# Performance work log

Hardware: AMD Instinct MI355X
Metric: run time of the kernel (lower is better)

Reference implementation:

```python
import jax, jax.numpy as jnp
import numpy as np

TOPK = 50
TEMP = 5.0

def _l2norm(x):
    return x / jnp.linalg.norm(x, axis=-1, keepdims=True)

def setup_inputs() -> dict:
    key = jax.random.key(0)
    k1, k2, k3 = jax.random.split(key, 3)
    b, m, d = 32, 196, 512
    n, c = 51, 1000
    return {
        "image_features": jax.random.normal(k1, (b, d), dtype=jnp.float32),
        "local_image_features": jax.random.normal(k2, (b, m, d), dtype=jnp.float32),
        "all_text_features": jax.random.normal(k3, (n, c, d), dtype=jnp.float32),
        "logit_scale": jnp.full((1,), 4.6052, dtype=jnp.float32),  # ln(100), CLIP default
    }

def reference(image_features, local_image_features, all_text_features, logit_scale):
    # Inference path of CustomCLIP.forward (labels=None) -> get_dense_logits2
    img = _l2norm(image_features)                 # [b, d]
    loc = _l2norm(local_image_features)           # [b, m, d]
    txt = _l2norm(all_text_features)              # [n, c, d]  (n = ndisc = 51)
    mean_txt = _l2norm(txt.mean(axis=0))          # [c, d]

    base_logits = img @ mean_txt.T                # [b, c]
    w_raw = jnp.einsum('bd,bmd->bm', img, loc)    # [b, m]
    txt_cnd = jnp.transpose(txt, (1, 0, 2))       # [c, n, d]
    v = jax.nn.softmax(jnp.einsum('cd,cnd->cn', mean_txt, txt_cnd) * TEMP, axis=1)  # [c, n]

    # similarity of every patch to every description, laid out with m last for top_k
    sim = jnp.einsum('bmd,cnd->bcnm', loc, txt_cnd)        # [b, c, n, m]
    sim_topk, idx_topk = jax.lax.top_k(sim, TOPK)          # [b, c, n, k] each

    b = img.shape[0]
    # gather per-image patch weights at selected patch indices: w_raw[b, idx]
    w_topk = w_raw[jnp.arange(b)[:, None, None, None], idx_topk]   # [b, c, n, k]
    w = jax.nn.softmax(w_topk * TEMP, axis=3)               # softmax over selected patches

    bias_logits = jnp.sum(sim_topk * w * v[None, :, :, None], axis=(2, 3))  # [b, c]
    return jnp.exp(logit_scale)[0] * (base_logits + bias_logits)
```

## Files before the change

kernel.cpp:

```cpp
#include <hip/hip_runtime.h>
#include <stdint.h>

typedef __bf16  bf16x8 __attribute__((ext_vector_type(8)));
typedef float   f32x4  __attribute__((ext_vector_type(4)));
typedef short   s16x2  __attribute__((ext_vector_type(2)));
typedef unsigned short u16;

#define TEMP 5.0f

__device__ inline float wsum(float v){
  #pragma unroll
  for (int off=32; off; off>>=1) v += __shfl_xor(v, off, 64);
  return v;
}
__device__ inline float wmax(float v){
  #pragma unroll
  for (int off=32; off; off>>=1) v = fmaxf(v, __shfl_xor(v, off, 64));
  return v;
}
__device__ inline u16 f2bf(float f){
  unsigned u = __float_as_uint(f);
  u = u + 0x7fffu + ((u>>16)&1u);
  return (u16)(u>>16);
}
__device__ inline float bfl(unsigned u){ return __uint_as_float(u<<16); }
__device__ inline float bfh(unsigned u){ return __uint_as_float(u & 0xffff0000u); }

__device__ inline s16x2 as_s16x2(int v){ union{int i; s16x2 v;} u; u.i=v; return u.v; }

__device__ inline s16x2 pkmin2(s16x2 a, s16x2 b){
  s16x2 r; r.x = a.x < b.x ? a.x : b.x; r.y = a.y < b.y ? a.y : b.y; return r;
}
__device__ inline s16x2 pkmax2(s16x2 a, s16x2 b){
  s16x2 r; r.x = a.x > b.x ? a.x : b.x; r.y = a.y > b.y ? a.y : b.y; return r;
}

#if __has_builtin(__builtin_amdgcn_mov_dpp)
__device__ inline int dxor1(int v){ return __builtin_amdgcn_mov_dpp(v, 0xB1, 0xF, 0xF, true); }
__device__ inline int dxor2(int v){ return __builtin_amdgcn_mov_dpp(v, 0x4E, 0xF, 0xF, true); }
#else
__device__ inline int dxor1(int v){ return __shfl_xor(v, 1, 64); }
__device__ inline int dxor2(int v){ return __shfl_xor(v, 2, 64); }
#endif

#if __has_builtin(__builtin_amdgcn_permlane16_swap)
__device__ inline int x16sum_i(int c){
  auto p = __builtin_amdgcn_permlane16_swap((unsigned)c, (unsigned)c, false, false);
  return (int)p[0] + (int)p[1];
}
__device__ inline int x16min_i(int c){
  auto p = __builtin_amdgcn_permlane16_swap((unsigned)c, (unsigned)c, false, false);
  return min((int)p[0], (int)p[1]);
}
__device__ inline int x16max_i(int c){
  auto p = __builtin_amdgcn_permlane16_swap((unsigned)c, (unsigned)c, false, false);
  return max((int)p[0], (int)p[1]);
}
__device__ inline float x16sum_f(float v){
  auto p = __builtin_amdgcn_permlane16_swap(__float_as_uint(v), __float_as_uint(v), false, false);
  return __uint_as_float(p[0]) + __uint_as_float(p[1]);
}
#else
__device__ inline int   x16sum_i(int c){ return c + __shfl_xor(c, 16, 64); }
__device__ inline int   x16min_i(int c){ return min(c, __shfl_xor(c, 16, 64)); }
__device__ inline int   x16max_i(int c){ return max(c, __shfl_xor(c, 16, 64)); }
__device__ inline float x16sum_f(float v){ return v + __shfl_xor(v, 16, 64); }
#endif

__device__ inline int ssum8_i(int c){ c += dxor1(c); c += dxor2(c); return x16sum_i(c); }
__device__ inline int smin8_i(int c){ c = min(c, dxor1(c)); c = min(c, dxor2(c)); return x16min_i(c); }
__device__ inline int smax8_i(int c){ c = max(c, dxor1(c)); c = max(c, dxor2(c)); return x16max_i(c); }
__device__ inline float ssum8_f(float v){
  v += __int_as_float(dxor1(__float_as_int(v)));
  v += __int_as_float(dxor2(__float_as_int(v)));
  return x16sum_f(v);
}

__device__ inline void cp16(void* lds_uniform, const void* g){
  __builtin_amdgcn_global_load_lds(
    (const __attribute__((address_space(1))) unsigned int*)g,
    (__attribute__((address_space(3))) unsigned int*)lds_uniform, 16, 0, 0);
}

__global__ void k_img(const float* __restrict__ X, float* __restrict__ imgn){
  int b = blockIdx.x, lane = threadIdx.x;
  const float* src = X + (size_t)b*512 + lane*8;
  float4 a = *(const float4*)src;
  float4 c = *(const float4*)(src+4);
  float ss = a.x*a.x+a.y*a.y+a.z*a.z+a.w*a.w + c.x*c.x+c.y*c.y+c.z*c.z+c.w*c.w;
  ss = wsum(ss);
  float inv = 1.0f/sqrtf(ss);
  float* dst = imgn + (size_t)b*512 + lane*8;
  float4 o0 = {a.x*inv,a.y*inv,a.z*inv,a.w*inv};
  float4 o1 = {c.x*inv,c.y*inv,c.z*inv,c.w*inv};
  *(float4*)dst = o0; *(float4*)(dst+4) = o1;
}

__global__ void k_txt(const float* __restrict__ X, u16* __restrict__ TXT, float* __restrict__ invn){
  int cn = blockIdx.x, lane = threadIdx.x;
  int kc = lane>>2, kk8 = (lane&3)*8;
  size_t dstE = ((size_t)kc*51008 + cn)*32 + kk8;
  if (cn >= 51000){
    uint4 z = {0,0,0,0};
    *(uint4*)(TXT + dstE) = z;
    return;
  }
  int c = cn/51, n = cn - c*51;
  const float* src = X + ((size_t)n*1000 + c)*512 + lane*8;
  float4 a = *(const float4*)src;
  float4 d = *(const float4*)(src+4);
  float ss = a.x*a.x+a.y*a.y+a.z*a.z+a.w*a.w + d.x*d.x+d.y*d.y+d.z*d.z+d.w*d.w;
  ss = wsum(ss);
  float inv = 1.0f/sqrtf(ss);
  u16 h0=f2bf(a.x*inv),h1=f2bf(a.y*inv),h2=f2bf(a.z*inv),h3=f2bf(a.w*inv);
  u16 h4=f2bf(d.x*inv),h5=f2bf(d.y*inv),h6=f2bf(d.z*inv),h7=f2bf(d.w*inv);
  uint4 o;
  o.x = (unsigned)h0 | ((unsigned)h1<<16);
  o.y = (unsigned)h2 | ((unsigned)h3<<16);
  o.z = (unsigned)h4 | ((unsigned)h5<<16);
  o.w = (unsigned)h6 | ((unsigned)h7<<16);
  *(uint4*)(TXT + dstE) = o;
  if (lane==0) invn[(size_t)n*1000 + c] = inv;
}

__global__ void k_mean(const float* __restrict__ X, const float* __restrict__ invn, float* __restrict__ MT){
  int c = blockIdx.x, tid = threadIdx.x, lane = tid&63, wv = tid>>6;
  __shared__ float sinv[51];
  __shared__ float red[4];
  if (tid < 51) sinv[tid] = invn[(size_t)tid*1000 + c];
  __syncthreads();
  int d0 = tid*2;
  float sx=0.f, sy=0.f;
  for (int n=0;n<51;++n){
    const float2 x = *(const float2*)(X + ((size_t)n*1000 + c)*512 + d0);
    float iv = sinv[n];
    sx += x.x*iv; sy += x.y*iv;
  }
  float ss = sx*sx + sy*sy;
  ss = wsum(ss);
  if (lane==0) red[wv] = ss;
  __syncthreads();
  float tot = red[0]+red[1]+red[2]+red[3];
  float inv = 1.0f/sqrtf(tot);
  float2 o = {sx*inv, sy*inv};
  *(float2*)(MT + (size_t)c*512 + d0) = o;
}

__global__ void k_v(const u16* __restrict__ TXT, const float* __restrict__ MT, float* __restrict__ vbuf){
  int c = blockIdx.x, lane = threadIdx.x;
  __shared__ float lg[51];
  const float* mp = MT + (size_t)c*512 + lane*8;
  float4 m0 = *(const float4*)mp;
  float4 m1 = *(const float4*)(mp+4);
  int kc = lane>>2, kk8 = (lane&3)*8;
  for (int n=0;n<51;++n){
    size_t e = ((size_t)kc*51008 + (size_t)(c*51+n))*32 + kk8;
    uint4 q = *(const uint4*)(TXT + e);
    float d = bfl(q.x)*m0.x + bfh(q.x)*m0.y + bfl(q.y)*m0.z + bfh(q.y)*m0.w
            + bfl(q.z)*m1.x + bfh(q.z)*m1.y + bfl(q.w)*m1.z + bfh(q.w)*m1.w;
    d = wsum(d);
    if (lane==0) lg[n] = d;
  }
  __syncthreads();
  float val = (lane<51) ? lg[lane] : -1e30f;
  float mx = wmax(val);
  float e = (lane<51) ? expf(TEMP*(val-mx)) : 0.f;
  float s = wsum(e);
  if (lane<51) vbuf[(size_t)c*51 + lane] = e/s;
}

__global__ void k_base(const float* __restrict__ imgn, const float* __restrict__ MT, float* __restrict__ bias){
  int c = blockIdx.x, lane = threadIdx.x;
  const float* mp = MT + (size_t)c*512 + lane*8;
  float4 m0 = *(const float4*)mp;
  float4 m1 = *(const float4*)(mp+4);
  for (int b=0;b<32;++b){
    const float* ip = imgn + (size_t)b*512 + lane*8;
    float4 i0 = *(const float4*)ip;
    float4 i1 = *(const float4*)(ip+4);
    float d = i0.x*m0.x+i0.y*m0.y+i0.z*m0.z+i0.w*m0.w
            + i1.x*m1.x+i1.y*m1.y+i1.z*m1.z+i1.w*m1.w;
    d = wsum(d);
    if (lane==0) bias[(size_t)b*1000 + c] = d;
  }
}

__global__ void k_loc(const float* __restrict__ L, const float* __restrict__ imgn,
                      u16* __restrict__ LOC, float* __restrict__ ewg){
  int m = blockIdx.x, b = blockIdx.y, lane = threadIdx.x;
  size_t dstE = ((size_t)(b*16 + (lane>>2))*224 + m)*32 + (lane&3)*8;
  if (m >= 196){
    uint4 z = {0,0,0,0};
    *(uint4*)(LOC + dstE) = z;
    if (lane==0) ewg[(size_t)b*224 + m] = 0.f;
    return;
  }
  const float* src = L + ((size_t)b*196 + m)*512 + lane*8;
  float4 a = *(const float4*)src;
  float4 d = *(const float4*)(src+4);
  const float* ip = imgn + (size_t)b*512 + lane*8;
  float4 i0 = *(const float4*)ip;
  float4 i1 = *(const float4*)(ip+4);
  float ss = a.x*a.x+a.y*a.y+a.z*a.z+a.w*a.w + d.x*d.x+d.y*d.y+d.z*d.z+d.w*d.w;
  float ws = a.x*i0.x+a.y*i0.y+a.z*i0.z+a.w*i0.w + d.x*i1.x+d.y*i1.y+d.z*i1.z+d.w*i1.w;
  ss = wsum(ss); ws = wsum(ws);
  float inv = 1.0f/sqrtf(ss);
  u16 h0=f2bf(a.x*inv),h1=f2bf(a.y*inv),h2=f2bf(a.z*inv),h3=f2bf(a.w*inv);
  u16 h4=f2bf(d.x*inv),h5=f2bf(d.y*inv),h6=f2bf(d.z*inv),h7=f2bf(d.w*inv);
  uint4 o;
  o.x = (unsigned)h0 | ((unsigned)h1<<16);
  o.y = (unsigned)h2 | ((unsigned)h3<<16);
  o.z = (unsigned)h4 | ((unsigned)h5<<16);
  o.w = (unsigned)h6 | ((unsigned)h7<<16);
  *(uint4*)(LOC + dstE) = o;
  if (lane==0) ewg[(size_t)b*224 + m] = expf(TEMP * ws * inv);
}

__global__ __launch_bounds__(512,8) void k_main(const u16* __restrict__ TXT, const u16* __restrict__ LOC,
                                                const float* __restrict__ ewg, const float* __restrict__ vbuf,
                                                float* __restrict__ bias){
  __shared__ __align__(16) char smem[30592];
  const int tid = threadIdx.x, lane = tid & 63, wv = tid >> 6;
  const int quad = lane >> 4, l16 = lane & 15;
  const int wm = wv >> 1, wn = wv & 1;
  const int NT = (wm == 3) ? 2 : 4;
  const int lsw = lane ^ ((lane>>3)&3);
  const int qsw = (quad ^ ((l16>>1)&3)) * 16;
  const int sub = (lane & 3) | ((lane >> 2) & 4);
  const int col = ((lane >> 2) & 3) | ((lane >> 3) & 4);

  int id = blockIdx.x, b, cnt_;
  if (id < 24576){
    int g = id >> 10, r = id & 1023;
    b = r >> 5;  cnt_ = (g << 5) + (r & 31);
  } else {
    int r = id - 24576;
    b = r / 29;  cnt_ = 768 + r % 29;
  }
  const int cn0 = cnt_ * 64;

  float* ewl = (float*)(smem + 29696);
  if (tid < 224) ewl[tid] = ewg[(size_t)b*224 + tid];

  const f32x4 zero = {0.f,0.f,0.f,0.f};
  f32x4 acc[4][2];
  #pragma unroll
  for (int t=0;t<4;++t){ acc[t][0]=zero; acc[t][1]=zero; }

  const u16* Abase = LOC + (size_t)(b*16)*224*32;
  char* Albd0 = smem;
  char* Albd1 = smem + 14336;

  auto stageA = [&](int kc, char* dst){
    const char* src = (const char*)(Abase + (size_t)kc*224*32);
    #pragma unroll
    for (int j=0;j<2;++j){
      int ch0 = j*512 + wv*64;
      if (ch0 < 896)
        cp16(dst + (size_t)ch0*16, src + (size_t)(ch0 + lsw)*16);
    }
  };
  struct B2 { bf16x8 x, y; };
  auto loadB = [&](int kc)->B2{
    B2 r;
    size_t e = ((size_t)kc*51008 + (size_t)(cn0 + 32*wn + l16))*32 + quad*8;
    r.x = *(const bf16x8*)(TXT + e);
    r.y = *(const bf16x8*)(TXT + e + 16*32);
    return r;
  };
  auto domfma = [&](const char* Ab, B2 bb){
    #pragma unroll
    for (int t=0;t<4;++t){
      if (t < NT){
        bf16x8 af = *(const bf16x8*)(Ab + (size_t)(((4*wm + t)*16 + l16)*64) + qsw);
        acc[t][0] = __builtin_amdgcn_mfma_f32_16x16x32_bf16(af, bb.x, acc[t][0], 0,0,0);
        acc[t][1] = __builtin_amdgcn_mfma_f32_16x16x32_bf16(af, bb.y, acc[t][1], 0,0,0);
      }
    }
  };

  stageA(0, Albd0);
  __syncthreads();

  for (int kc = 0; kc < 16; ++kc){
    char* cur = (kc & 1) ? Albd1 : Albd0;
    char* nxt = (kc & 1) ? Albd0 : Albd1;
    B2 bb = loadB(kc);
    if (kc < 15) stageA(kc+1, nxt);
    domfma(cur, bb);
    __syncthreads();
  }

  const float KSC = 15360.0f;
  {
    #pragma unroll
    for (int n=0;n<2;++n){
      unsigned* wr = (unsigned*)(void*)smem + (size_t)((2*wn + n)*1856) + l16*116 + quad*2;
      #pragma unroll
      for (int t=0;t<4;++t){
        if (t < NT){
          int a0 = (int)(acc[t][n][0]*KSC), a1 = (int)(acc[t][n][1]*KSC);
          int a2 = (int)(acc[t][n][2]*KSC), a3 = (int)(acc[t][n][3]*KSC);
          uint2 o; o.x = (unsigned)((a0 & 0xffff) | (a1<<16)); o.y = (unsigned)((a2 & 0xffff) | (a3<<16));
          *(uint2*)(wr + (4*wm + t)*8) = o;
        }
      }
    }
  }
  __syncthreads();

  int kk[7][2];
  {
    const unsigned* rd = (const unsigned*)(void*)smem + (size_t)((wv>>1)*1856) + ((wv&1)*8 + col)*116 + sub*14;
    #pragma unroll
    for (int j=0;j<7;++j){
      uint2 q = *(const uint2*)(rd + 2*j);
      kk[j][0] = (int)q.x;
      kk[j][1] = (int)q.y;
    }
  }
  const int PKPK = (int)0xC180C180;
  if (sub == 7){
    #pragma unroll
    for (int j=0;j<7;++j){ kk[j][0] = PKPK; kk[j][1] = PKPK; }
  }

  s16x2 vmn = as_s16x2(kk[0][0]), vmx = vmn;
  #pragma unroll
  for (int j=0;j<7;++j){
    #pragma unroll
    for (int i=0;i<2;++i){
      vmn = pkmin2(vmn, as_s16x2(kk[j][i]));
      vmx = pkmax2(vmx, as_s16x2(kk[j][i]));
    }
  }
  int kmn = min((int)vmn.x, (int)vmn.y);
  int kmx = max((int)vmx.x, (int)vmx.y);
  if (sub == 7){ kmn = 32000; kmx = -32000; }
  kmn = smin8_i(kmn);
  kmx = smax8_i(kmx);
  int lo = kmn - 1, hi = kmx + 1;

  float flo = 146.0f, fhi = -50.0f;
  int side = 0;
  bool done = false;

  #pragma unroll 1
  for (int it = 0; it < 14; ++it){
    float fr = flo * __builtin_amdgcn_rcpf(flo - fhi);
    fr = fminf(fmaxf(fr, 0.04f), 0.96f);
    int tm = lo + (int)(fr * (float)(hi - lo));
    tm = (tm <= lo) ? (lo + 1) : ((tm >= hi) ? (hi - 1) : tm);

    s16x2 tmv = as_s16x2((tm & 0xffff) | (tm << 16));
    s16x2 ca = {0,0};
    #pragma unroll
    for (int j=0;j<7;++j){
      ca = ca + ((as_s16x2(kk[j][0]) - tmv) >> 15);
      ca = ca + ((as_s16x2(kk[j][1]) - tmv) >> 15);
    }
    int clt = -((int)ca.x + (int)ca.y);
    int c = ssum8_i(28 - clt);

    bool ge = (c >= 50);
    if (!done){
      if (ge){ fhi = (side==1)  ? fhi*0.5f : fhi; flo = (float)(c-50); lo = tm; side = 1; }
      else   { flo = (side==-1) ? flo*0.5f : flo; fhi = (float)(c-50); hi = tm; side = -1; }
    }
    done = done || (c == 50) || ((hi - lo) <= 1);
    if (__all(done)) break;
  }
  const int thr = lo;

  float num = 0.f, den = 0.f;
  #pragma unroll
  for (int j=0;j<7;++j){
    float2 e0 = *(const float2*)(ewl + 28*sub + 4*j);
    float2 e1 = *(const float2*)(ewl + 28*sub + 4*j + 2);
    int a0 = (kk[j][0]<<16)>>16, a1 = kk[j][0]>>16;
    int a2 = (kk[j][1]<<16)>>16, a3 = kk[j][1]>>16;
    if (a0 >= thr){ num = fmaf((float)a0, e0.x, num); den += e0.x; }
    if (a1 >= thr){ num = fmaf((float)a1, e0.y, num); den += e0.y; }
    if (a2 >= thr){ num = fmaf((float)a2, e1.x, num); den += e1.x; }
    if (a3 >= thr){ num = fmaf((float)a3, e1.y, num); den += e1.y; }
  }
  num = ssum8_f(num);
  den = ssum8_f(den);

  int cn = cn0 + (wv>>1)*16 + (wv&1)*8 + col;
  if (sub == 0 && cn < 51000){
    int c = cn/51;
    atomicAdd(bias + (size_t)b*1000 + c, vbuf[cn]*(num/(den*KSC)));
  }
}

__global__ void k_out(const float* __restrict__ bias, const float* __restrict__ ls, float* __restrict__ out){
  int i = blockIdx.x*256 + threadIdx.x;
  if (i < 32000){
    float sc = expf(ls[0]);
    out[i] = sc * bias[i];
  }
}

extern "C" void kernel_launch(void* const* d_in, const int* in_sizes, int n_in,
                              void* d_out, int out_size, void* d_ws, size_t ws_size,
                              hipStream_t stream) {
  const float* img = (const float*)d_in[0];
  const float* loc = (const float*)d_in[1];
  const float* txt = (const float*)d_in[2];
  const float* ls  = (const float*)d_in[3];
  char* ws = (char*)d_ws;
  float* imgn = (float*)(ws + 0);
  float* MT   = (float*)(ws + 65536);
  float* invn = (float*)(ws + 2113536);
  float* vbuf = (float*)(ws + 2317568);
  float* ewg  = (float*)(ws + 2521600);
  float* bias = (float*)(ws + 2550272);
  u16*   TXT  = (u16*)  (ws + 2678272);
  u16*   LOC  = (u16*)  (ws + 54910464);

  k_img <<<dim3(32),      dim3(64),  0, stream>>>(img, imgn);
  k_txt <<<dim3(51008),   dim3(64),  0, stream>>>(txt, TXT, invn);
  k_mean<<<dim3(1000),    dim3(256), 0, stream>>>(txt, invn, MT);
  k_v   <<<dim3(1000),    dim3(64),  0, stream>>>(TXT, MT, vbuf);
  k_base<<<dim3(1000),    dim3(64),  0, stream>>>(imgn, MT, bias);
  k_loc <<<dim3(224,32),  dim3(64),  0, stream>>>(loc, imgn, LOC, ewg);
  k_main<<<dim3(25504),   dim3(512), 0, stream>>>(TXT, LOC, ewg, vbuf, bias);
  k_out <<<dim3(125),     dim3(256), 0, stream>>>(bias, ls, (float*)d_out);
}
```

Baseline: 996.7 us.

## Load MFMA A fragments directly from global memory instead of LDS double-buffering

```diff
diff --git a/kernel.cpp b/kernel.cpp
--- a/kernel.cpp
+++ b/kernel.cpp
@@ -74,12 +74,6 @@
   v += __int_as_float(dxor1(__float_as_int(v)));
   v += __int_as_float(dxor2(__float_as_int(v)));
   return x16sum_f(v);
-}
-
-__device__ inline void cp16(void* lds_uniform, const void* g){
-  __builtin_amdgcn_global_load_lds(
-    (const __attribute__((address_space(1))) unsigned int*)g,
-    (__attribute__((address_space(3))) unsigned int*)lds_uniform, 16, 0, 0);
 }
 
 __global__ void k_img(const float* __restrict__ X, float* __restrict__ imgn){
@@ -223,9 +217,6 @@
   const int tid = threadIdx.x, lane = tid & 63, wv = tid >> 6;
   const int quad = lane >> 4, l16 = lane & 15;
   const int wm = wv >> 1, wn = wv & 1;
-  const int NT = (wm == 3) ? 2 : 4;
-  const int lsw = lane ^ ((lane>>3)&3);
-  const int qsw = (quad ^ ((l16>>1)&3)) * 16;
   const int sub = (lane & 3) | ((lane >> 2) & 4);
   const int col = ((lane >> 2) & 3) | ((lane >> 3) & 4);
 
@@ -247,50 +238,44 @@
   #pragma unroll
   for (int t=0;t<4;++t){ acc[t][0]=zero; acc[t][1]=zero; }
 
-  const u16* Abase = LOC + (size_t)(b*16)*224*32;
-  char* Albd0 = smem;
-  char* Albd1 = smem + 14336;
-
-  auto stageA = [&](int kc, char* dst){
-    const char* src = (const char*)(Abase + (size_t)kc*224*32);
-    #pragma unroll
-    for (int j=0;j<2;++j){
-      int ch0 = j*512 + wv*64;
-      if (ch0 < 896)
-        cp16(dst + (size_t)ch0*16, src + (size_t)(ch0 + lsw)*16);
-    }
-  };
-  struct B2 { bf16x8 x, y; };
-  auto loadB = [&](int kc)->B2{
-    B2 r;
-    size_t e = ((size_t)kc*51008 + (size_t)(cn0 + 32*wn + l16))*32 + quad*8;
-    r.x = *(const bf16x8*)(TXT + e);
-    r.y = *(const bf16x8*)(TXT + e + 16*32);
-    return r;
-  };
-  auto domfma = [&](const char* Ab, B2 bb){
-    #pragma unroll
-    for (int t=0;t<4;++t){
-      if (t < NT){
-        bf16x8 af = *(const bf16x8*)(Ab + (size_t)(((4*wm + t)*16 + l16)*64) + qsw);
-        acc[t][0] = __builtin_amdgcn_mfma_f32_16x16x32_bf16(af, bb.x, acc[t][0], 0,0,0);
-        acc[t][1] = __builtin_amdgcn_mfma_f32_16x16x32_bf16(af, bb.y, acc[t][1], 0,0,0);
-      }
-    }
-  };
-
-  stageA(0, Albd0);
-  __syncthreads();
-
-  for (int kc = 0; kc < 16; ++kc){
-    char* cur = (kc & 1) ? Albd1 : Albd0;
-    char* nxt = (kc & 1) ? Albd0 : Albd1;
-    B2 bb = loadB(kc);
-    if (kc < 15) stageA(kc+1, nxt);
-    domfma(cur, bb);
-    __syncthreads();
-  }
-
+  const u16* Aw = LOC + (size_t)(b*16)*7168 + (size_t)((64*wm + l16))*32 + quad*8;
+  const u16* Bw = TXT + (size_t)(cn0 + 32*wn + l16)*32 + quad*8;
+
+  if (wm != 3){
+    for (int kc = 0; kc < 16; ++kc){
+      const u16* ak = Aw + (size_t)kc*7168;
+      const u16* bk = Bw + (size_t)kc*(51008*32);
+      bf16x8 bx  = *(const bf16x8*)(bk);
+      bf16x8 by  = *(const bf16x8*)(bk + 512);
+      bf16x8 af0 = *(const bf16x8*)(ak);
+      bf16x8 af1 = *(const bf16x8*)(ak + 512);
+      bf16x8 af2 = *(const bf16x8*)(ak + 1024);
+      bf16x8 af3 = *(const bf16x8*)(ak + 1536);
+      acc[0][0] = __builtin_amdgcn_mfma_f32_16x16x32_bf16(af0, bx, acc[0][0], 0,0,0);
+      acc[0][1] = __builtin_amdgcn_mfma_f32_16x16x32_bf16(af0, by, acc[0][1], 0,0,0);
+      acc[1][0] = __builtin_amdgcn_mfma_f32_16x16x32_bf16(af1, bx, acc[1][0], 0,0,0);
+      acc[1][1] = __builtin_amdgcn_mfma_f32_16x16x32_bf16(af1, by, acc[1][1], 0,0,0);
+      acc[2][0] = __builtin_amdgcn_mfma_f32_16x16x32_bf16(af2, bx, acc[2][0], 0,0,0);
+      acc[2][1] = __builtin_amdgcn_mfma_f32_16x16x32_bf16(af2, by, acc[2][1], 0,0,0);
+      acc[3][0] = __builtin_amdgcn_mfma_f32_16x16x32_bf16(af3, bx, acc[3][0], 0,0,0);
+      acc[3][1] = __builtin_amdgcn_mfma_f32_16x16x32_bf16(af3, by, acc[3][1], 0,0,0);
+    }
+  } else {
+    for (int kc = 0; kc < 16; ++kc){
+      const u16* ak = Aw + (size_t)kc*7168;
+      const u16* bk = Bw + (size_t)kc*(51008*32);
+      bf16x8 bx  = *(const bf16x8*)(bk);
+      bf16x8 by  = *(const bf16x8*)(bk + 512);
+      bf16x8 af0 = *(const bf16x8*)(ak);
+      bf16x8 af1 = *(const bf16x8*)(ak + 512);
+      acc[0][0] = __builtin_amdgcn_mfma_f32_16x16x32_bf16(af0, bx, acc[0][0], 0,0,0);
+      acc[0][1] = __builtin_amdgcn_mfma_f32_16x16x32_bf16(af0, by, acc[0][1], 0,0,0);
+      acc[1][0] = __builtin_amdgcn_mfma_f32_16x16x32_bf16(af1, bx, acc[1][0], 0,0,0);
+      acc[1][1] = __builtin_amdgcn_mfma_f32_16x16x32_bf16(af1, by, acc[1][1], 0,0,0);
+    }
+  }
+
+  const int NT = (wm == 3) ? 2 : 4;
   const float KSC = 15360.0f;
   {
     #pragma unroll
```

After: 1.391 ms. 39.5% more time.
